# Kernel optimization log

Hardware: AMD Instinct MI355X
Metric: run time of the kernel (lower is better)

Reference implementation:

```python
import jax, jax.numpy as jnp
import numpy as np

B, M, V = 16, 1024, 4
ALPHA_T, ALPHA_S, ALPHA_TS = 0.5, 0.75, 0.5


def setup_inputs() -> dict:
    key = jax.random.key(0)
    k1, k2 = jax.random.split(key)
    pred_dT = jax.random.normal(k1, (B, M, M, 4), dtype=jnp.float32)
    gt_dT = jax.random.normal(k2, (B, M, M, 4), dtype=jnp.float32)
    # V views, each contributing M // V tokens (sum(Ms) == M)
    Ms = jnp.full((V,), M // V, dtype=jnp.int32)
    return {"pred_dT": pred_dT, "gt_dT": gt_dT, "Ms": Ms}


def reference(pred_dT, gt_dT, Ms):
    Bv, Mv = pred_dT.shape[:2]
    Vv = Ms.shape[0]
    # view id of each of the M tokens: [0]*Ms[0] ++ [1]*Ms[1] ++ ...
    view_ids = jnp.repeat(jnp.arange(Vv), Ms, total_repeat_length=Mv)  # [M]
    # inter-view mask over token pairs
    inter = (view_ids[None, :] != view_ids[:, None]).astype(pred_dT.dtype)  # [M, M]

    # mse, reduction='none', then split channels: 0:2 -> t, 2:4 -> s
    diff = (pred_dT - gt_dT) ** 2  # [B, M, M, 4]
    t = diff[..., 0] + diff[..., 1]  # [B, M, M]
    s = diff[..., 2] + diff[..., 3]  # [B, M, M]

    inter_t = jnp.sum(t * inter)
    inter_s = jnp.sum(s * inter)
    intra_t = jnp.sum(t) - inter_t
    intra_s = jnp.sum(s) - inter_s

    sum_Ms_sq = jnp.sum(Ms * Ms).astype(pred_dT.dtype)
    diag_count = sum_Ms_sq * Bv
    offdiag_count = (Mv * Mv - sum_Ms_sq) * Bv

    loss_intra_t = intra_t / diag_count
    loss_intra_s = intra_s / diag_count
    loss_inter_t = inter_t / offdiag_count
    loss_inter_s = inter_s / offdiag_count

    loss_t = ALPHA_T * loss_inter_t + (1.0 - ALPHA_T) * loss_intra_t
    loss_s = ALPHA_S * loss_inter_s + (1.0 - ALPHA_S) * loss_intra_s
    loss = ALPHA_TS * loss_t + (1.0 - ALPHA_TS) * loss_s

    # order: intra_t, inter_t, intra_s, inter_s, loss_t, loss_s, loss
    return jnp.stack([loss_intra_t, loss_inter_t, loss_intra_s,
                      loss_inter_s, loss_t, loss_s, loss])
```

## Files before the change

### kernel.cpp

```cpp
#include <hip/hip_runtime.h>

#define M_DIM 1024
#define M_SHIFT 10
#define BLOCK 256
#define GRID 2048


__global__ void pose_loss_partial(const float4* __restrict__ pred,
                                  const float4* __restrict__ gt,
                                  const int* __restrict__ Ms, int V,
                                  long long N, float4* __restrict__ part)
{
    int cum[9];
    cum[0] = 0;
#pragma unroll
    for (int v = 0; v < 8; ++v) {
        int m = (v < V) ? Ms[v] : 0;
        cum[v + 1] = cum[v] + m;
    }

    float tt = 0.f, ss = 0.f, it = 0.f, is = 0.f;

    const long long stride = (long long)gridDim.x * BLOCK;
    for (long long idx = (long long)blockIdx.x * BLOCK + threadIdx.x;
         idx < N; idx += stride) {
        int j = (int)(idx & (M_DIM - 1));
        int i = (int)((idx >> M_SHIFT) & (M_DIM - 1));

        float4 p = pred[idx];
        float4 g = gt[idx];
        float d0 = p.x - g.x, d1 = p.y - g.y, d2 = p.z - g.z, d3 = p.w - g.w;
        float t = d0 * d0 + d1 * d1;
        float s = d2 * d2 + d3 * d3;

        int vi = 0, vj = 0;
#pragma unroll
        for (int v = 1; v < 8; ++v) {
            if (v < V) {
                vi += (i >= cum[v]);
                vj += (j >= cum[v]);
            }
        }
        float w = (vi != vj) ? 1.0f : 0.0f;
        tt += t;
        ss += s;
        it += t * w;
        is += s * w;
    }

#pragma unroll
    for (int off = 32; off > 0; off >>= 1) {
        tt += __shfl_down(tt, off);
        ss += __shfl_down(ss, off);
        it += __shfl_down(it, off);
        is += __shfl_down(is, off);
    }

    __shared__ float l_tt[BLOCK / 64], l_ss[BLOCK / 64],
                     l_it[BLOCK / 64], l_is[BLOCK / 64];
    int wave = threadIdx.x >> 6;
    int lane = threadIdx.x & 63;
    if (lane == 0) {
        l_tt[wave] = tt; l_ss[wave] = ss;
        l_it[wave] = it; l_is[wave] = is;
    }
    __syncthreads();
    if (threadIdx.x == 0) {
        float a = 0.f, b = 0.f, c = 0.f, d = 0.f;
#pragma unroll
        for (int w = 0; w < BLOCK / 64; ++w) {
            a += l_tt[w]; b += l_ss[w]; c += l_it[w]; d += l_is[w];
        }
        part[blockIdx.x] = make_float4(a, b, c, d);
    }
}

__global__ void pose_loss_final(const float4* __restrict__ part, int nparts,
                                const int* __restrict__ Ms, int V, int B,
                                float* __restrict__ out)
{
    double tt = 0.0, ss = 0.0, it = 0.0, is = 0.0;
    for (int k = threadIdx.x; k < nparts; k += BLOCK) {
        float4 q = part[k];
        tt += q.x; ss += q.y; it += q.z; is += q.w;
    }
#pragma unroll
    for (int off = 32; off > 0; off >>= 1) {
        tt += __shfl_down(tt, off);
        ss += __shfl_down(ss, off);
        it += __shfl_down(it, off);
        is += __shfl_down(is, off);
    }
    __shared__ double l_tt[BLOCK / 64], l_ss[BLOCK / 64],
                      l_it[BLOCK / 64], l_is[BLOCK / 64];
    int wave = threadIdx.x >> 6;
    int lane = threadIdx.x & 63;
    if (lane == 0) {
        l_tt[wave] = tt; l_ss[wave] = ss;
        l_it[wave] = it; l_is[wave] = is;
    }
    __syncthreads();
    if (threadIdx.x == 0) {
        double s_tt = 0, s_ss = 0, s_it = 0, s_is = 0;
#pragma unroll
        for (int w = 0; w < BLOCK / 64; ++w) {
            s_tt += l_tt[w]; s_ss += l_ss[w];
            s_it += l_it[w]; s_is += l_is[w];
        }
        long long sumsq = 0;
        for (int v = 0; v < V; ++v) {
            long long m = Ms[v];
            sumsq += m * m;
        }
        double diag = (double)sumsq * (double)B;
        double offd = ((double)M_DIM * (double)M_DIM - (double)sumsq) * (double)B;

        double li_t = (s_tt - s_it) / diag;
        double le_t = s_it / offd;
        double li_s = (s_ss - s_is) / diag;
        double le_s = s_is / offd;

        const double A_T = 0.5, A_S = 0.75, A_TS = 0.5;
        double lt = A_T * le_t + (1.0 - A_T) * li_t;
        double ls = A_S * le_s + (1.0 - A_S) * li_s;
        double loss = A_TS * lt + (1.0 - A_TS) * ls;

        out[0] = (float)li_t;
        out[1] = (float)le_t;
        out[2] = (float)li_s;
        out[3] = (float)le_s;
        out[4] = (float)lt;
        out[5] = (float)ls;
        out[6] = (float)loss;
    }
}

extern "C" void kernel_launch(void* const* d_in, const int* in_sizes, int n_in,
                              void* d_out, int out_size, void* d_ws, size_t ws_size,
                              hipStream_t stream)
{
    const float* pred = (const float*)d_in[0];
    const float* gt   = (const float*)d_in[1];
    const int*   Ms   = (const int*)d_in[2];
    int V = in_sizes[2];

    long long total = (long long)in_sizes[0];
    long long N     = total / 4;
    int B           = (int)(total / (4LL * M_DIM * M_DIM));

    float4* part = (float4*)d_ws;

    pose_loss_partial<<<GRID, BLOCK, 0, stream>>>(
        (const float4*)pred, (const float4*)gt, Ms, V, N, part);
    pose_loss_final<<<1, BLOCK, 0, stream>>>(part, GRID, Ms, V, B,
                                             (float*)d_out);
}
```

Before: 504.5 us.

## Unroll partial reduction into chunked loads with hoisted view-id computation

```diff
diff --git a/kernel.cpp b/kernel.cpp
--- a/kernel.cpp
+++ b/kernel.cpp
@@ -4,12 +4,15 @@
 #define M_SHIFT 10
 #define BLOCK 256
 #define GRID 2048
-
-
-__global__ void pose_loss_partial(const float4* __restrict__ pred,
-                                  const float4* __restrict__ gt,
-                                  const int* __restrict__ Ms, int V,
-                                  long long N, float4* __restrict__ part)
+#define UNROLL 8
+#define CHUNK (BLOCK * UNROLL)
+
+
+__global__ __launch_bounds__(BLOCK, 4)
+void pose_loss_partial(const float4* __restrict__ pred,
+                       const float4* __restrict__ gt,
+                       const int* __restrict__ Ms, int V,
+                       long long N, float4* __restrict__ part)
 {
     int cum[9];
     cum[0] = 0;
@@ -19,33 +22,86 @@
         cum[v + 1] = cum[v] + m;
     }
 
+    const int t = threadIdx.x;
+
+    int vj[4];
+#pragma unroll
+    for (int q = 0; q < 4; ++q) {
+        int j = q * BLOCK + t;
+        int vid = 0;
+#pragma unroll
+        for (int v = 1; v < 8; ++v)
+            if (v < V) vid += (j >= cum[v]);
+        vj[q] = vid;
+    }
+
     float tt = 0.f, ss = 0.f, it = 0.f, is = 0.f;
 
-    const long long stride = (long long)gridDim.x * BLOCK;
-    for (long long idx = (long long)blockIdx.x * BLOCK + threadIdx.x;
-         idx < N; idx += stride) {
-        int j = (int)(idx & (M_DIM - 1));
-        int i = (int)((idx >> M_SHIFT) & (M_DIM - 1));
-
+    const long long nchunks = N / CHUNK;
+    for (long long c = blockIdx.x; c < nchunks; c += gridDim.x) {
+        const long long base = c * CHUNK;
+
+        const int i0 = (int)((c * 2) & (M_DIM - 1));
+        int vi0 = 0, vi1 = 0;
+#pragma unroll
+        for (int v = 1; v < 8; ++v) {
+            if (v < V) {
+                vi0 += (i0 >= cum[v]);
+                vi1 += (i0 + 1 >= cum[v]);
+            }
+        }
+
+        float w[UNROLL];
+#pragma unroll
+        for (int q = 0; q < 4; ++q) {
+            w[q]     = (vj[q] != vi0) ? 1.0f : 0.0f;
+            w[q + 4] = (vj[q] != vi1) ? 1.0f : 0.0f;
+        }
+
+        float4 p[UNROLL], g[UNROLL];
+#pragma unroll
+        for (int k = 0; k < UNROLL; ++k) {
+            const long long off = base + k * BLOCK + t;
+            p[k] = pred[off];
+            g[k] = gt[off];
+        }
+#pragma unroll
+        for (int k = 0; k < UNROLL; ++k) {
+            const float d0 = p[k].x - g[k].x;
+            const float d1 = p[k].y - g[k].y;
+            const float d2 = p[k].z - g[k].z;
+            const float d3 = p[k].w - g[k].w;
+            const float tv = d0 * d0 + d1 * d1;
+            const float sv = d2 * d2 + d3 * d3;
+            tt += tv;
+            ss += sv;
+            it = fmaf(tv, w[k], it);
+            is = fmaf(sv, w[k], is);
+        }
+    }
+
+    for (long long idx = nchunks * CHUNK + (long long)blockIdx.x * BLOCK + t;
+         idx < N; idx += (long long)gridDim.x * BLOCK) {
+        const int j = (int)(idx & (M_DIM - 1));
+        const int i = (int)((idx >> M_SHIFT) & (M_DIM - 1));
         float4 p = pred[idx];
         float4 g = gt[idx];
         float d0 = p.x - g.x, d1 = p.y - g.y, d2 = p.z - g.z, d3 = p.w - g.w;
-        float t = d0 * d0 + d1 * d1;
-        float s = d2 * d2 + d3 * d3;
-
-        int vi = 0, vj = 0;
+        float tv = d0 * d0 + d1 * d1;
+        float sv = d2 * d2 + d3 * d3;
+        int vi = 0, vjj = 0;
 #pragma unroll
         for (int v = 1; v < 8; ++v) {
             if (v < V) {
                 vi += (i >= cum[v]);
-                vj += (j >= cum[v]);
+                vjj += (j >= cum[v]);
             }
         }
-        float w = (vi != vj) ? 1.0f : 0.0f;
-        tt += t;
-        ss += s;
-        it += t * w;
-        is += s * w;
+        float wv = (vi != vjj) ? 1.0f : 0.0f;
+        tt += tv;
+        ss += sv;
+        it = fmaf(tv, wv, it);
+        is = fmaf(sv, wv, is);
     }
 
 #pragma unroll
@@ -66,12 +122,12 @@
     }
     __syncthreads();
     if (threadIdx.x == 0) {
-        float a = 0.f, b = 0.f, c = 0.f, d = 0.f;
-#pragma unroll
-        for (int w = 0; w < BLOCK / 64; ++w) {
-            a += l_tt[w]; b += l_ss[w]; c += l_it[w]; d += l_is[w];
-        }
-        part[blockIdx.x] = make_float4(a, b, c, d);
+        float a = 0.f, b = 0.f, cc = 0.f, d = 0.f;
+#pragma unroll
+        for (int w2 = 0; w2 < BLOCK / 64; ++w2) {
+            a += l_tt[w2]; b += l_ss[w2]; cc += l_it[w2]; d += l_is[w2];
+        }
+        part[blockIdx.x] = make_float4(a, b, cc, d);
     }
 }
 
```

New measurement: 507.6 us. No clear change (+0.6%).
